# Kernel optimization log

Hardware: AMD Instinct MI355X
Metric: run time of the kernel (lower is better)

Reference implementation:

```python
import jax, jax.numpy as jnp
import numpy as np
import math

IN_DIM = 256
HID_DIM = 256
NUM_EDGE_TYPES = 3
HEADS = 8
HEAD_DIM = HID_DIM // HEADS  # 32
QK_DIM = (NUM_EDGE_TYPES + 1) * HID_DIM  # 1024
N = 4096


def _glorot(key, shape):
    # torch_geometric-style glorot: uniform(-a, a), a = sqrt(6/(fan_in+fan_out)) over last two dims
    a = math.sqrt(6.0 / (shape[-2] + shape[-1]))
    return jax.random.uniform(key, shape, jnp.float32, -a, a)


def setup_inputs() -> dict:
    key = jax.random.key(0)
    ks = jax.random.split(key, 8)
    return {
        "input_x": jax.random.normal(ks[0], (N, IN_DIM), jnp.float32),
        "pe_Q": jax.random.normal(ks[1], (N, NUM_EDGE_TYPES * HID_DIM), jnp.float32),
        "pe_K": jax.random.normal(ks[2], (N, NUM_EDGE_TYPES * HID_DIM), jnp.float32),
        "A": jnp.zeros((N, N), jnp.int32),  # accepted by forward but unused
        "WQ": _glorot(ks[3], (HEADS, QK_DIM, HEAD_DIM)),
        "WK": _glorot(ks[4], (HEADS, QK_DIM, HEAD_DIM)),
        "WV": _glorot(ks[5], (HEADS, IN_DIM, HEAD_DIM)),
        "Q_bias": jnp.zeros((HEADS, 1, HEAD_DIM), jnp.float32),
        "K_bias": jnp.zeros((HEADS, 1, HEAD_DIM), jnp.float32),
        "V_bias": jnp.zeros((HEADS, 1, HEAD_DIM), jnp.float32),
        "lin_w": _glorot(ks[6], (HID_DIM, HID_DIM)),
        "lin_b": jnp.zeros((HID_DIM,), jnp.float32),
    }


def reference(input_x, pe_Q, pe_K, A, WQ, WK, WV, Q_bias, K_bias, V_bias, lin_w, lin_b):
    x_Q = jnp.concatenate([input_x, pe_Q], axis=-1)  # [N, QK_DIM]
    x_K = jnp.concatenate([input_x, pe_K], axis=-1)  # [N, QK_DIM]
    Q = jnp.einsum('nd,hdk->hnk', x_Q, WQ) + Q_bias   # [H, N, hd]
    K = jnp.einsum('nd,hdk->hnk', x_K, WK) + K_bias   # [H, N, hd]
    V = jnp.einsum('nd,hdk->hnk', input_x, WV) + V_bias
    scores = jnp.einsum('hnk,hmk->hnm', Q, K) / math.sqrt(HID_DIM)  # [H, N, N]
    scores = scores - jax.lax.stop_gradient(jnp.max(scores, axis=-1, keepdims=True))
    attn = jax.nn.softmax(scores, axis=-1)
    attn = jnp.where(jnp.isnan(attn), jnp.zeros_like(attn), attn)
    attn_x = jnp.einsum('hnm,hmk->hnk', attn, V)      # [H, N, hd]
    # cat(list over heads, dim=1) -> [N, H*hd] with head-major column order
    x_cat = jnp.transpose(attn_x, (1, 0, 2)).reshape(attn_x.shape[1], -1)
    return x_cat @ lin_w.T + lin_b
```

## Files before the change

### kernel.cpp

```cpp
#include <hip/hip_runtime.h>
#include <hip/hip_bf16.h>

typedef __attribute__((ext_vector_type(8))) short bf16x8;
typedef __attribute__((ext_vector_type(4))) float f32x4;

__device__ __forceinline__ unsigned short f2b(float f) {
    union { float f; unsigned int u; } v; v.f = f;
    unsigned int u = v.u;
    unsigned int r = (u + 0x7FFFu + ((u >> 16) & 1u)) >> 16;
    return (unsigned short)r;
}
__device__ __forceinline__ float b2f(unsigned short h) {
    union { unsigned int u; float f; } v; v.u = ((unsigned int)h) << 16;
    return v.f;
}
__device__ __forceinline__ unsigned pk2(float a, float b) {
    union { __hip_bfloat162 h; unsigned u; } c;
    c.h = __float22bfloat162_rn(make_float2(a, b));
    return c.u;
}

__global__ __launch_bounds__(256) void prep_w(
    const float* __restrict__ WQ, const float* __restrict__ WK,
    const float* __restrict__ WV,
    const float* __restrict__ Qb, const float* __restrict__ Kb,
    const float* __restrict__ Vb,
    unsigned short* __restrict__ WQt, unsigned short* __restrict__ WKt,
    unsigned short* __restrict__ WVt,
    unsigned short* __restrict__ Bq, unsigned short* __restrict__ Bk,
    unsigned short* __restrict__ Bv) {
    int b = blockIdx.x, t = threadIdx.x;
    if (b < 288) {
        const float* W; unsigned short* Wt; int h, d0, D; float sc = 1.0f;
        if (b < 128)      { W = WQ; Wt = WQt; h = b >> 4;   d0 = (b & 15) * 64; D = 1024; sc = 0.0625f; }
        else if (b < 256) { int bb = b - 128; W = WK; Wt = WKt; h = bb >> 4; d0 = (bb & 15) * 64; D = 1024; }
        else              { int bb = b - 256; W = WV; Wt = WVt; h = bb >> 2; d0 = (bb & 3) * 64;  D = 256; }
        __shared__ float Ts[32][65];
        int dr = t >> 2, k0 = (t & 3) * 8;
        const float* src = W + (h * D + d0 + dr) * 32 + k0;
        float4 u0 = *(const float4*)src;
        float4 u1 = *(const float4*)(src + 4);
        Ts[k0 + 0][dr] = u0.x; Ts[k0 + 1][dr] = u0.y; Ts[k0 + 2][dr] = u0.z; Ts[k0 + 3][dr] = u0.w;
        Ts[k0 + 4][dr] = u1.x; Ts[k0 + 5][dr] = u1.y; Ts[k0 + 6][dr] = u1.z; Ts[k0 + 7][dr] = u1.w;
        __syncthreads();
        int k = t >> 3, dc = (t & 7) * 8;
        union { unsigned short s[8]; uint4 v; } pk;
#pragma unroll
        for (int i = 0; i < 8; i++) pk.s[i] = f2b(Ts[k][dc + i] * sc);
        *(uint4*)(Wt + (h * 32 + k) * D + d0 + dc) = pk.v;
    } else {
        Bq[t] = f2b(Qb[t] * 0.0625f); Bk[t] = f2b(Kb[t]); Bv[t] = f2b(Vb[t]);
    }
}

__global__ __launch_bounds__(256) void proj_fused(
    const float* __restrict__ x,
    const float* __restrict__ peQ, const float* __restrict__ peK,
    const unsigned short* __restrict__ WQt, const unsigned short* __restrict__ WKt,
    const unsigned short* __restrict__ WVt,
    const unsigned short* __restrict__ Bq, const unsigned short* __restrict__ Bk,
    const unsigned short* __restrict__ Bv,
    unsigned short* __restrict__ Qc, unsigned short* __restrict__ Kc,
    unsigned short* __restrict__ Vtr) {
    __shared__ unsigned short As[64 * 72];
    __shared__ unsigned short Bs[64 * 72];
    int bx = blockIdx.x;
    int which = bx >> 8, bb = bx & 255;
    const float* A1; const unsigned short* Bt; const unsigned short* bias; int K;
    if (which == 0)      { A1 = peQ; Bt = WQt; bias = Bq; K = 1024; }
    else if (which == 1) { A1 = peK; Bt = WKt; bias = Bk; K = 1024; }
    else                 { A1 = peQ; Bt = WVt; bias = Bv; K = 256; }
    int mb = bb & 63, nb = bb >> 6;
    int m0 = mb * 64, n0 = nb * 64;
    int t = threadIdx.x, w = t >> 6, lane = t & 63;
    int ln = lane & 15, q8 = (lane >> 4) * 8;
    int wm = (w >> 1) * 32, wn = (w & 1) * 32;
    int sr = t >> 3, sc = (t & 7) * 8;
    f32x4 acc[2][2];
#pragma unroll
    for (int i = 0; i < 2; i++)
#pragma unroll
        for (int j = 0; j < 2; j++) acc[i][j] = (f32x4){0.f, 0.f, 0.f, 0.f};
    for (int kb = 0; kb < K; kb += 64) {
#pragma unroll
        for (int half = 0; half < 2; half++) {
            int r = sr + half * 32;
            int c = kb + sc;
            const float* ap = (c < 256)
                ? (x + (m0 + r) * 256 + c)
                : (A1 + (m0 + r) * 768 + (c - 256));
            float4 u0 = *(const float4*)ap;
            float4 u1 = *(const float4*)(ap + 4);
            union { unsigned u[4]; uint4 v; } pk;
            pk.u[0] = pk2(u0.x, u0.y); pk.u[1] = pk2(u0.z, u0.w);
            pk.u[2] = pk2(u1.x, u1.y); pk.u[3] = pk2(u1.z, u1.w);
            *(uint4*)&As[r * 72 + sc] = pk.v;
            *(uint4*)&Bs[r * 72 + sc] = *(const uint4*)(Bt + (n0 + r) * K + c);
        }
        __syncthreads();
#pragma unroll
        for (int ks = 0; ks < 64; ks += 32) {
            bf16x8 a[2], b[2];
#pragma unroll
            for (int i = 0; i < 2; i++) {
                a[i] = *(const bf16x8*)&As[(wm + i * 16 + ln) * 72 + ks + q8];
                b[i] = *(const bf16x8*)&Bs[(wn + i * 16 + ln) * 72 + ks + q8];
            }
#pragma unroll
            for (int i = 0; i < 2; i++)
#pragma unroll
                for (int j = 0; j < 2; j++)
                    acc[i][j] = __builtin_amdgcn_mfma_f32_16x16x32_bf16(a[i], b[j], acc[i][j], 0, 0, 0);
        }
        __syncthreads();
    }
#pragma unroll
    for (int j = 0; j < 2; j++) {
        int ncol = n0 + wn + j * 16 + ln;
        float bv = b2f(bias[ncol]);
#pragma unroll
        for (int i = 0; i < 2; i++) {
            int rbase = m0 + wm + i * 16 + ((lane >> 4) * 4);
            if (which < 2) {
                unsigned short* C = which ? Kc : Qc;
#pragma unroll
                for (int r = 0; r < 4; r++)
                    C[(rbase + r) * 256 + ncol] = f2b(acc[i][j][r] + bv);
            } else {
                unsigned lo = pk2(acc[i][j][0] + bv, acc[i][j][1] + bv);
                unsigned hi = pk2(acc[i][j][2] + bv, acc[i][j][3] + bv);
                uint2 vv; vv.x = lo; vv.y = hi;
                *(uint2*)(Vtr + ncol * 4096 + rbase) = vv;
            }
        }
    }
}

__global__ __launch_bounds__(256, 3) void attn_kernel(
    const unsigned short* __restrict__ Qc,
    const unsigned short* __restrict__ Kc,
    const unsigned short* __restrict__ Vt,
    unsigned short* __restrict__ Xc) {
    __shared__ float Om[4][32][33];
    __shared__ float Ls[4][32];
    int head = blockIdx.x >> 7;
    int qb = blockIdx.x & 127;
    int t = threadIdx.x, w = t >> 6, lane = t & 63;
    int ln = lane & 15, quad = lane >> 4, q8 = quad * 8;
    int q0 = qb * 32;
    bf16x8 qfv[2];
#pragma unroll
    for (int qf = 0; qf < 2; qf++)
        qfv[qf] = *(const bf16x8*)(Qc + (q0 + qf * 16 + ln) * 256 + head * 32 + q8);
    const unsigned short* kbase[4];
#pragma unroll
    for (int kt = 0; kt < 4; kt++) {
        int key = 8 * (ln >> 2) + (ln & 3) + 4 * (kt & 1) + 32 * (kt >> 1);
        kbase[kt] = Kc + key * 256 + head * 32 + q8;
    }
    const unsigned short* vb0 = Vt + (head * 32 + ln) * 4096 + q8;
    const unsigned short* vb1 = Vt + (head * 32 + 16 + ln) * 4096 + q8;
    f32x4 o[2][2];
#pragma unroll
    for (int qf = 0; qf < 2; qf++)
#pragma unroll
        for (int hh = 0; hh < 2; hh++) o[qf][hh] = (f32x4){0.f, 0.f, 0.f, 0.f};
    const f32x4 z = {0.f, 0.f, 0.f, 0.f};
    f32x4 lacc[2]; lacc[0] = z; lacc[1] = z;
    int base = w * 1024;
    bf16x8 k0 = *(const bf16x8*)(kbase[0] + base * 256);
    bf16x8 k1 = *(const bf16x8*)(kbase[1] + base * 256);
    bf16x8 k2 = *(const bf16x8*)(kbase[2] + base * 256);
    bf16x8 k3 = *(const bf16x8*)(kbase[3] + base * 256);
    bf16x8 v0 = *(const bf16x8*)(vb0 + base);
    bf16x8 v1 = *(const bf16x8*)(vb0 + base + 32);
    bf16x8 v2 = *(const bf16x8*)(vb1 + base);
    bf16x8 v3 = *(const bf16x8*)(vb1 + base + 32);
#pragma unroll 1
    for (int it = 0; it < 16; it++) {
        int nit = (it < 15) ? (it + 1) : 15;
        int nkb = base + nit * 64;
        bf16x8 nk0 = *(const bf16x8*)(kbase[0] + nkb * 256);
        bf16x8 nk1 = *(const bf16x8*)(kbase[1] + nkb * 256);
        bf16x8 nk2 = *(const bf16x8*)(kbase[2] + nkb * 256);
        bf16x8 nk3 = *(const bf16x8*)(kbase[3] + nkb * 256);
        bf16x8 nv0 = *(const bf16x8*)(vb0 + nkb);
        bf16x8 nv1 = *(const bf16x8*)(vb0 + nkb + 32);
        bf16x8 nv2 = *(const bf16x8*)(vb1 + nkb);
        bf16x8 nv3 = *(const bf16x8*)(vb1 + nkb + 32);
#pragma unroll
        for (int qf = 0; qf < 2; qf++) {
            f32x4 s0 = __builtin_amdgcn_mfma_f32_16x16x32_bf16(k0, qfv[qf], z, 0, 0, 0);
            f32x4 s1 = __builtin_amdgcn_mfma_f32_16x16x32_bf16(k1, qfv[qf], z, 0, 0, 0);
            f32x4 s2 = __builtin_amdgcn_mfma_f32_16x16x32_bf16(k2, qfv[qf], z, 0, 0, 0);
            f32x4 s3 = __builtin_amdgcn_mfma_f32_16x16x32_bf16(k3, qfv[qf], z, 0, 0, 0);
            float p0[4], p1[4], p2[4], p3[4];
#pragma unroll
            for (int r = 0; r < 4; r++) {
                p0[r] = __expf(s0[r]); p1[r] = __expf(s1[r]);
                p2[r] = __expf(s2[r]); p3[r] = __expf(s3[r]);
            }
            f32x4 ps;
#pragma unroll
            for (int r = 0; r < 4; r++) ps[r] = (p0[r] + p1[r]) + (p2[r] + p3[r]);
            lacc[qf] += ps;
            union { unsigned u[4]; bf16x8 v; } b0, b1;
            b0.u[0] = pk2(p0[0], p0[1]); b0.u[1] = pk2(p0[2], p0[3]);
            b0.u[2] = pk2(p1[0], p1[1]); b0.u[3] = pk2(p1[2], p1[3]);
            b1.u[0] = pk2(p2[0], p2[1]); b1.u[1] = pk2(p2[2], p2[3]);
            b1.u[2] = pk2(p3[0], p3[1]); b1.u[3] = pk2(p3[2], p3[3]);
            o[qf][0] = __builtin_amdgcn_mfma_f32_16x16x32_bf16(v0, b0.v, o[qf][0], 0, 0, 0);
            o[qf][0] = __builtin_amdgcn_mfma_f32_16x16x32_bf16(v1, b1.v, o[qf][0], 0, 0, 0);
            o[qf][1] = __builtin_amdgcn_mfma_f32_16x16x32_bf16(v2, b0.v, o[qf][1], 0, 0, 0);
            o[qf][1] = __builtin_amdgcn_mfma_f32_16x16x32_bf16(v3, b1.v, o[qf][1], 0, 0, 0);
        }
        k0 = nk0; k1 = nk1; k2 = nk2; k3 = nk3;
        v0 = nv0; v1 = nv1; v2 = nv2; v3 = nv3;
    }
#pragma unroll
    for (int qf = 0; qf < 2; qf++) {
        float lts = (lacc[qf][0] + lacc[qf][1]) + (lacc[qf][2] + lacc[qf][3]);
        lts += __shfl_xor(lts, 16, 64);
        lts += __shfl_xor(lts, 32, 64);
#pragma unroll
        for (int r = 0; r < 4; r++) {
            Om[w][quad * 4 + r][qf * 16 + ln] = o[qf][0][r];
            Om[w][16 + quad * 4 + r][qf * 16 + ln] = o[qf][1][r];
        }
        if (quad == 0) Ls[w][qf * 16 + ln] = lts;
    }
    __syncthreads();
    int q = t & 31, d = (t >> 5) * 4;
    float num[4] = {0.f, 0.f, 0.f, 0.f};
    float den = 0.f;
#pragma unroll
    for (int w2 = 0; w2 < 4; w2++) {
        den += Ls[w2][q];
#pragma unroll
        for (int i = 0; i < 4; i++) num[i] += Om[w2][d + i][q];
    }
    float inv = 1.f / den;
    uint2 outv;
    outv.x = pk2(num[0] * inv, num[1] * inv);
    outv.y = pk2(num[2] * inv, num[3] * inv);
    *(uint2*)(Xc + (q0 + q) * 256 + head * 32 + d) = outv;
}

__global__ __launch_bounds__(256) void gemm_out(
    const unsigned short* __restrict__ A,
    const float* __restrict__ LW,
    const float* __restrict__ Lb,
    float* __restrict__ C) {
    __shared__ unsigned short As[64 * 72];
    __shared__ unsigned short Bs[64 * 72];
    int mb = blockIdx.x & 63, nb = blockIdx.x >> 6;
    int m0 = mb * 64, n0 = nb * 64;
    int t = threadIdx.x, w = t >> 6, lane = t & 63;
    int ln = lane & 15, q8 = (lane >> 4) * 8;
    int wm = (w >> 1) * 32, wn = (w & 1) * 32;
    int sr = t >> 3, sc = (t & 7) * 8;
    f32x4 acc[2][2];
#pragma unroll
    for (int i = 0; i < 2; i++)
#pragma unroll
        for (int j = 0; j < 2; j++) acc[i][j] = (f32x4){0.f, 0.f, 0.f, 0.f};
    for (int kb = 0; kb < 256; kb += 64) {
#pragma unroll
        for (int half = 0; half < 2; half++) {
            int r = sr + half * 32;
            int c = kb + sc;
            *(uint4*)&As[r * 72 + sc] = *(const uint4*)(A + (m0 + r) * 256 + c);
            const float* bp = LW + (n0 + r) * 256 + c;
            float4 u0 = *(const float4*)bp;
            float4 u1 = *(const float4*)(bp + 4);
            union { unsigned u[4]; uint4 v; } pk;
            pk.u[0] = pk2(u0.x, u0.y); pk.u[1] = pk2(u0.z, u0.w);
            pk.u[2] = pk2(u1.x, u1.y); pk.u[3] = pk2(u1.z, u1.w);
            *(uint4*)&Bs[r * 72 + sc] = pk.v;
        }
        __syncthreads();
#pragma unroll
        for (int ks = 0; ks < 64; ks += 32) {
            bf16x8 a[2], b[2];
#pragma unroll
            for (int i = 0; i < 2; i++) {
                a[i] = *(const bf16x8*)&As[(wm + i * 16 + ln) * 72 + ks + q8];
                b[i] = *(const bf16x8*)&Bs[(wn + i * 16 + ln) * 72 + ks + q8];
            }
#pragma unroll
            for (int i = 0; i < 2; i++)
#pragma unroll
                for (int j = 0; j < 2; j++)
                    acc[i][j] = __builtin_amdgcn_mfma_f32_16x16x32_bf16(a[i], b[j], acc[i][j], 0, 0, 0);
        }
        __syncthreads();
    }
#pragma unroll
    for (int j = 0; j < 2; j++) {
        int ncol = n0 + wn + j * 16 + ln;
        float bv = Lb[ncol];
#pragma unroll
        for (int i = 0; i < 2; i++) {
            int rbase = m0 + wm + i * 16 + ((lane >> 4) * 4);
#pragma unroll
            for (int r = 0; r < 4; r++)
                C[(rbase + r) * 256 + ncol] = acc[i][j][r] + bv;
        }
    }
}

extern "C" void kernel_launch(void* const* d_in, const int* in_sizes, int n_in,
                              void* d_out, int out_size, void* d_ws, size_t ws_size,
                              hipStream_t stream) {
    const float* input_x = (const float*)d_in[0];
    const float* pe_Q    = (const float*)d_in[1];
    const float* pe_K    = (const float*)d_in[2];
    const float* WQ = (const float*)d_in[4];
    const float* WK = (const float*)d_in[5];
    const float* WV = (const float*)d_in[6];
    const float* Qb = (const float*)d_in[7];
    const float* Kb = (const float*)d_in[8];
    const float* Vb = (const float*)d_in[9];
    const float* lw = (const float*)d_in[10];
    const float* lb = (const float*)d_in[11];

    unsigned short* ws = (unsigned short*)d_ws;
    unsigned short* WQt = ws;
    unsigned short* WKt = WQt + 262144;
    unsigned short* WVt = WKt + 262144;
    unsigned short* Bq  = WVt + 65536;
    unsigned short* Bk  = Bq + 256;
    unsigned short* Bv  = Bk + 256;
    unsigned short* Qc  = Bv + 256;
    unsigned short* Kc  = Qc + 1048576;
    unsigned short* Vtr = Kc + 1048576;
    unsigned short* Xc  = Vtr + 1048576;

    prep_w<<<dim3(289), dim3(256), 0, stream>>>(WQ, WK, WV, Qb, Kb, Vb,
                                                WQt, WKt, WVt, Bq, Bk, Bv);
    proj_fused<<<dim3(768), dim3(256), 0, stream>>>(input_x, pe_Q, pe_K,
                                                    WQt, WKt, WVt, Bq, Bk, Bv,
                                                    Qc, Kc, Vtr);
    attn_kernel<<<dim3(1024), dim3(256), 0, stream>>>(Qc, Kc, Vtr, Xc);
    gemm_out<<<dim3(256), dim3(256), 0, stream>>>(Xc, lw, lb, (float*)d_out);
}
```

Baseline: 212.6 us.

## Pre-swizzle K and V into per-head fragment-ordered tiles for contiguous attention loads

The projection kernel now writes K and V into one interleaved buffer laid out per head and per 64-key tile, in the exact order the MFMA fragments are consumed. Each lane of the attention kernel can then load its K and V operands with fully contiguous 16-byte reads at fixed offsets, replacing strided row gathers. The attention launch bound is raised to allow four blocks per CU. In exchange, the projection epilogue does scattered scalar stores for K and takes on more complex index math.

```diff
diff --git a/kernel.cpp b/kernel.cpp
--- a/kernel.cpp
+++ b/kernel.cpp
@@ -19,6 +19,7 @@
     c.h = __float22bfloat162_rn(make_float2(a, b));
     return c.u;
 }
+
 
 __global__ __launch_bounds__(256) void prep_w(
     const float* __restrict__ WQ, const float* __restrict__ WK,
@@ -60,8 +61,7 @@
     const unsigned short* __restrict__ WVt,
     const unsigned short* __restrict__ Bq, const unsigned short* __restrict__ Bk,
     const unsigned short* __restrict__ Bv,
-    unsigned short* __restrict__ Qc, unsigned short* __restrict__ Kc,
-    unsigned short* __restrict__ Vtr) {
+    unsigned short* __restrict__ Qc, unsigned short* __restrict__ KV) {
     __shared__ unsigned short As[64 * 72];
     __shared__ unsigned short Bs[64 * 72];
     int bx = blockIdx.x;
@@ -118,28 +118,43 @@
     for (int j = 0; j < 2; j++) {
         int ncol = n0 + wn + j * 16 + ln;
         float bv = b2f(bias[ncol]);
+        int h2 = ncol >> 5, din = ncol & 31;
 #pragma unroll
         for (int i = 0; i < 2; i++) {
             int rbase = m0 + wm + i * 16 + ((lane >> 4) * 4);
-            if (which < 2) {
-                unsigned short* C = which ? Kc : Qc;
+            if (which == 0) {
 #pragma unroll
                 for (int r = 0; r < 4; r++)
-                    C[(rbase + r) * 256 + ncol] = f2b(acc[i][j][r] + bv);
+                    Qc[(rbase + r) * 256 + ncol] = f2b(acc[i][j][r] + bv);
+            } else if (which == 1) {
+#pragma unroll
+                for (int r = 0; r < 4; r++) {
+                    int key = rbase + r;
+                    int T2 = key >> 6, k6 = key & 63;
+                    int kt = ((k6 >> 2) & 1) + ((k6 >> 4) & 2);
+                    int ln2 = ((k6 >> 3) & 3) * 4 + (k6 & 3);
+                    int addr = (h2 * 64 + T2) * 4096 + kt * 512
+                             + ((din >> 3) * 16 + ln2) * 8 + (din & 7);
+                    KV[addr] = f2b(acc[i][j][r] + bv);
+                }
             } else {
-                unsigned lo = pk2(acc[i][j][0] + bv, acc[i][j][1] + bv);
-                unsigned hi = pk2(acc[i][j][2] + bv, acc[i][j][3] + bv);
-                uint2 vv; vv.x = lo; vv.y = hi;
-                *(uint2*)(Vtr + ncol * 4096 + rbase) = vv;
+                int key = rbase;
+                int T2 = key >> 6, k6 = key & 63;
+                int chunk = 4 + ((din >> 4) << 1) + ((k6 >> 5) & 1);
+                int lane2 = ((k6 >> 3) & 3) * 16 + (din & 15);
+                int addr = (h2 * 64 + T2) * 4096 + chunk * 512 + lane2 * 8 + (k6 & 7);
+                uint2 vv;
+                vv.x = pk2(acc[i][j][0] + bv, acc[i][j][1] + bv);
+                vv.y = pk2(acc[i][j][2] + bv, acc[i][j][3] + bv);
+                *(uint2*)(KV + addr) = vv;
             }
         }
     }
 }
 
-__global__ __launch_bounds__(256, 3) void attn_kernel(
+__global__ __launch_bounds__(256, 4) void attn_kernel(
     const unsigned short* __restrict__ Qc,
-    const unsigned short* __restrict__ Kc,
-    const unsigned short* __restrict__ Vt,
+    const unsigned short* __restrict__ KV,
     unsigned short* __restrict__ Xc) {
     __shared__ float Om[4][32][33];
     __shared__ float Ls[4][32];
@@ -152,14 +167,7 @@
 #pragma unroll
     for (int qf = 0; qf < 2; qf++)
         qfv[qf] = *(const bf16x8*)(Qc + (q0 + qf * 16 + ln) * 256 + head * 32 + q8);
-    const unsigned short* kbase[4];
-#pragma unroll
-    for (int kt = 0; kt < 4; kt++) {
-        int key = 8 * (ln >> 2) + (ln & 3) + 4 * (kt & 1) + 32 * (kt >> 1);
-        kbase[kt] = Kc + key * 256 + head * 32 + q8;
-    }
-    const unsigned short* vb0 = Vt + (head * 32 + ln) * 4096 + q8;
-    const unsigned short* vb1 = Vt + (head * 32 + 16 + ln) * 4096 + q8;
+    const unsigned short* kv = KV + (head * 64 + w * 16) * 4096 + lane * 8;
     f32x4 o[2][2];
 #pragma unroll
     for (int qf = 0; qf < 2; qf++)
@@ -167,27 +175,26 @@
         for (int hh = 0; hh < 2; hh++) o[qf][hh] = (f32x4){0.f, 0.f, 0.f, 0.f};
     const f32x4 z = {0.f, 0.f, 0.f, 0.f};
     f32x4 lacc[2]; lacc[0] = z; lacc[1] = z;
-    int base = w * 1024;
-    bf16x8 k0 = *(const bf16x8*)(kbase[0] + base * 256);
-    bf16x8 k1 = *(const bf16x8*)(kbase[1] + base * 256);
-    bf16x8 k2 = *(const bf16x8*)(kbase[2] + base * 256);
-    bf16x8 k3 = *(const bf16x8*)(kbase[3] + base * 256);
-    bf16x8 v0 = *(const bf16x8*)(vb0 + base);
-    bf16x8 v1 = *(const bf16x8*)(vb0 + base + 32);
-    bf16x8 v2 = *(const bf16x8*)(vb1 + base);
-    bf16x8 v3 = *(const bf16x8*)(vb1 + base + 32);
+    bf16x8 k0 = *(const bf16x8*)(kv + 0);
+    bf16x8 k1 = *(const bf16x8*)(kv + 512);
+    bf16x8 k2 = *(const bf16x8*)(kv + 1024);
+    bf16x8 k3 = *(const bf16x8*)(kv + 1536);
+    bf16x8 v0 = *(const bf16x8*)(kv + 2048);
+    bf16x8 v1 = *(const bf16x8*)(kv + 2560);
+    bf16x8 v2 = *(const bf16x8*)(kv + 3072);
+    bf16x8 v3 = *(const bf16x8*)(kv + 3584);
 #pragma unroll 1
     for (int it = 0; it < 16; it++) {
         int nit = (it < 15) ? (it + 1) : 15;
-        int nkb = base + nit * 64;
-        bf16x8 nk0 = *(const bf16x8*)(kbase[0] + nkb * 256);
-        bf16x8 nk1 = *(const bf16x8*)(kbase[1] + nkb * 256);
-        bf16x8 nk2 = *(const bf16x8*)(kbase[2] + nkb * 256);
-        bf16x8 nk3 = *(const bf16x8*)(kbase[3] + nkb * 256);
-        bf16x8 nv0 = *(const bf16x8*)(vb0 + nkb);
-        bf16x8 nv1 = *(const bf16x8*)(vb0 + nkb + 32);
-        bf16x8 nv2 = *(const bf16x8*)(vb1 + nkb);
-        bf16x8 nv3 = *(const bf16x8*)(vb1 + nkb + 32);
+        const unsigned short* nkv = kv + nit * 4096;
+        bf16x8 nk0 = *(const bf16x8*)(nkv + 0);
+        bf16x8 nk1 = *(const bf16x8*)(nkv + 512);
+        bf16x8 nk2 = *(const bf16x8*)(nkv + 1024);
+        bf16x8 nk3 = *(const bf16x8*)(nkv + 1536);
+        bf16x8 nv0 = *(const bf16x8*)(nkv + 2048);
+        bf16x8 nv1 = *(const bf16x8*)(nkv + 2560);
+        bf16x8 nv2 = *(const bf16x8*)(nkv + 3072);
+        bf16x8 nv3 = *(const bf16x8*)(nkv + 3584);
 #pragma unroll
         for (int qf = 0; qf < 2; qf++) {
             f32x4 s0 = __builtin_amdgcn_mfma_f32_16x16x32_bf16(k0, qfv[qf], z, 0, 0, 0);
@@ -332,15 +339,14 @@
     unsigned short* Bk  = Bq + 256;
     unsigned short* Bv  = Bk + 256;
     unsigned short* Qc  = Bv + 256;
-    unsigned short* Kc  = Qc + 1048576;
-    unsigned short* Vtr = Kc + 1048576;
-    unsigned short* Xc  = Vtr + 1048576;
+    unsigned short* KVb = Qc + 1048576;
+    unsigned short* Xc  = KVb + 2097152;
 
     prep_w<<<dim3(289), dim3(256), 0, stream>>>(WQ, WK, WV, Qb, Kb, Vb,
                                                 WQt, WKt, WVt, Bq, Bk, Bv);
     proj_fused<<<dim3(768), dim3(256), 0, stream>>>(input_x, pe_Q, pe_K,
                                                     WQt, WKt, WVt, Bq, Bk, Bv,
-                                                    Qc, Kc, Vtr);
-    attn_kernel<<<dim3(1024), dim3(256), 0, stream>>>(Qc, Kc, Vtr, Xc);
+                                                    Qc, KVb);
+    attn_kernel<<<dim3(1024), dim3(256), 0, stream>>>(Qc, KVb, Xc);
     gemm_out<<<dim3(256), dim3(256), 0, stream>>>(Xc, lw, lb, (float*)d_out);
 }
```

Result: faster. 181.9 us (-14.4%).
